# Optimization experiments

Measured on AMD Instinct MI355X. Metric: run time of the kernel, lower is better.

## Reference

```python
import jax, jax.numpy as jnp
import numpy as np

B, N, M, D = 16, 4096, 4096, 3


def setup_inputs() -> dict:
    key = jax.random.key(0)
    k1, k2 = jax.random.split(key)
    xyz1 = jax.random.normal(k1, (B, N, D), dtype=jnp.float32)
    xyz2 = jax.random.normal(k2, (B, M, D), dtype=jnp.float32)
    return {"xyz1": xyz1, "xyz2": xyz2}


def _chamfer(xyz1, xyz2):
    # Squared pairwise distances via ||a||^2 + ||b||^2 - 2 a.b  -> [B, N, M]
    s1 = jnp.sum(xyz1 * xyz1, axis=-1)                     # [B, N]
    s2 = jnp.sum(xyz2 * xyz2, axis=-1)                     # [B, M]
    cross = jnp.einsum("bnd,bmd->bnm", xyz1, xyz2)        # [B, N, M]
    d2 = s1[:, :, None] + s2[:, None, :] - 2.0 * cross
    d2 = jnp.maximum(d2, 0.0)  # guard tiny negatives from cancellation
    dist1 = jnp.min(d2, axis=2)  # nearest point in set2 for each point in set1, [B, N]
    dist2 = jnp.min(d2, axis=1)  # nearest point in set1 for each point in set2, [B, M]
    return dist1, dist2


def reference(xyz1, xyz2):
    return _chamfer(xyz1, xyz2)
```

## Files before the change

### kernel.cpp

```cpp
#include <hip/hip_runtime.h>

typedef _Float16 h8     __attribute__((ext_vector_type(8)));
typedef float    f32x16 __attribute__((ext_vector_type(16)));

#define BB      16
#define NPTS    4096
#define WAVES   4
#define RPW     64
#define RPB     (WAVES * RPW)
#define CSPLIT  2
#define COLS    (NPTS / CSPLIT)
#define CHUNK   256
#define NCHUNK  (COLS / CHUNK)
#define NT      (CHUNK / 32)
#define TPB     (WAVES * 64)

__global__ __launch_bounds__(256) void chamfer_init_out(float* __restrict__ out) {
    int i = blockIdx.x * 256 + threadIdx.x;
    out[i] = 3.0e38f;
}

__global__ __launch_bounds__(TPB, 4) void chamfer_mfma(
    const float* __restrict__ xyz1,
    const float* __restrict__ xyz2,
    float* __restrict__ out)
{
    __shared__ __align__(16) _Float16 sb[2][CHUNK * 16];

    const int tid  = threadIdx.x;
    const int lane = tid & 63;
    const int wv   = tid >> 6;
    const int rb   = blockIdx.x;
    const int b    = blockIdx.y;
    const int z    = blockIdx.z;
    const int dir  = z & 1;
    const int csp  = z >> 1;

    const float* qbase = (dir == 0 ? xyz1 : xyz2) + b * NPTS * 3;
    const float* dbase = (dir == 0 ? xyz2 : xyz1) + b * NPTS * 3 + csp * COLS * 3;

    h8 af0, af1;
#pragma unroll
    for (int rbi = 0; rbi < 2; ++rbi) {
        const int row = rb * RPB + wv * RPW + rbi * 32 + (lane & 31);
        float x = qbase[row * 3 + 0], y = qbase[row * 3 + 1], z2 = qbase[row * 3 + 2];
        float s = fmaf(x, x, fmaf(y, y, z2 * z2));
        _Float16 xh = (_Float16)x, yh = (_Float16)y, zh = (_Float16)z2;
        _Float16 xl = (_Float16)(x - (float)xh);
        _Float16 yl = (_Float16)(y - (float)yh);
        _Float16 zl = (_Float16)(z2 - (float)zh);
        _Float16 sh = (_Float16)s;
        _Float16 sl = (_Float16)(s - (float)sh);
        _Float16 one = (_Float16)1.0f, zero = (_Float16)0.0f;
        h8 a = (lane < 32) ? h8{xh, yh, zh, xh, yh, zh, xl, yl}
                           : h8{zl, sh, sl, one, one, zero, zero, zero};
        if (rbi == 0) af0 = a; else af1 = a;
    }

    const f32x16 Z = {};
    float rm0[16], rm1[16];
#pragma unroll
    for (int r = 0; r < 16; ++r) { rm0[r] = 3.0e38f; rm1[r] = 3.0e38f; }

    const int loff = ((lane >> 5) << 8) + (lane & 31) * 8;

    float vx, vy, vz;
    auto stage_load = [&](int ch) {
        const float* p = dbase + (ch * CHUNK + tid) * 3;
        vx = p[0]; vy = p[1]; vz = p[2];
    };
    auto stage_write = [&](int buf) {
        float s = fmaf(vx, vx, fmaf(vy, vy, vz * vz));
        _Float16 xh = (_Float16)vx, yh = (_Float16)vy, zh = (_Float16)vz;
        _Float16 m2xh = (_Float16)(-2.0f) * xh;
        _Float16 m2yh = (_Float16)(-2.0f) * yh;
        _Float16 m2zh = (_Float16)(-2.0f) * zh;
        _Float16 m2xl = (_Float16)(-2.0f * (vx - (float)xh));
        _Float16 m2yl = (_Float16)(-2.0f * (vy - (float)yh));
        _Float16 m2zl = (_Float16)(-2.0f * (vz - (float)zh));
        _Float16 sh = (_Float16)s;
        _Float16 sl = (_Float16)(s - (float)sh);
        _Float16 one = (_Float16)1.0f, zero = (_Float16)0.0f;
        int off = (tid >> 5) * 512 + (tid & 31) * 8;
        *(h8*)&sb[buf][off]       = h8{m2xh, m2yh, m2zh, m2xl, m2yl, m2zl, m2xh, m2yh};
        *(h8*)&sb[buf][off + 256] = h8{m2zh, one, one, sh, sl, zero, zero, zero};
    };

#define FOLD0(p) _Pragma("unroll") for (int r = 0; r < 16; ++r) rm0[r] = fminf((p)[r], rm0[r]);
#define FOLD1(p) _Pragma("unroll") for (int r = 0; r < 16; ++r) rm1[r] = fminf((p)[r], rm1[r]);

    auto sweep = [&](int buf) {
        const _Float16* base = &sb[buf][0];
        h8 b0 = *(const h8*)(base + loff);
        f32x16 pA0 = __builtin_amdgcn_mfma_f32_32x32x16_f16(af0, b0, Z, 0, 0, 0);
        f32x16 pA1 = __builtin_amdgcn_mfma_f32_32x32x16_f16(af1, b0, Z, 0, 0, 0);
#pragma unroll 1
        for (int t = 1; t + 1 < NT; t += 2) {
            h8 bx = *(const h8*)(base + t * 512 + loff);
            f32x16 pB0 = __builtin_amdgcn_mfma_f32_32x32x16_f16(af0, bx, Z, 0, 0, 0);
            FOLD0(pA0)
            f32x16 pB1 = __builtin_amdgcn_mfma_f32_32x32x16_f16(af1, bx, Z, 0, 0, 0);
            FOLD1(pA1)
            h8 by = *(const h8*)(base + (t + 1) * 512 + loff);
            pA0 = __builtin_amdgcn_mfma_f32_32x32x16_f16(af0, by, Z, 0, 0, 0);
            FOLD0(pB0)
            pA1 = __builtin_amdgcn_mfma_f32_32x32x16_f16(af1, by, Z, 0, 0, 0);
            FOLD1(pB1)
        }
        {
            h8 bx = *(const h8*)(base + (NT - 1) * 512 + loff);
            f32x16 pB0 = __builtin_amdgcn_mfma_f32_32x32x16_f16(af0, bx, Z, 0, 0, 0);
            FOLD0(pA0)
            f32x16 pB1 = __builtin_amdgcn_mfma_f32_32x32x16_f16(af1, bx, Z, 0, 0, 0);
            FOLD1(pA1)
            FOLD0(pB0)
            FOLD1(pB1)
        }
    };

    stage_load(0);
    stage_write(0);
    __syncthreads();
#pragma unroll 1
    for (int ch = 0; ch < NCHUNK; ++ch) {
        int buf = ch & 1;
        if (ch + 1 < NCHUNK) stage_load(ch + 1);
        sweep(buf);
        if (ch + 1 < NCHUNK) stage_write(buf ^ 1);
        __syncthreads();
    }

#pragma unroll
    for (int r = 0; r < 16; ++r) {
        float m = rm0[r];
        m = fminf(m, __shfl_xor(m, 1));
        m = fminf(m, __shfl_xor(m, 2));
        m = fminf(m, __shfl_xor(m, 4));
        m = fminf(m, __shfl_xor(m, 8));
        m = fminf(m, __shfl_xor(m, 16));
        rm0[r] = m;
        float n = rm1[r];
        n = fminf(n, __shfl_xor(n, 1));
        n = fminf(n, __shfl_xor(n, 2));
        n = fminf(n, __shfl_xor(n, 4));
        n = fminf(n, __shfl_xor(n, 8));
        n = fminf(n, __shfl_xor(n, 16));
        rm1[r] = n;
    }
    if ((lane & 31) == 0) {
        const int half = lane >> 5;
        int* o = (int*)out + dir * (BB * NPTS) + b * NPTS + rb * RPB + wv * RPW;
#pragma unroll
        for (int r = 0; r < 16; ++r) {
            int rr = (r & 3) + 8 * (r >> 2) + 4 * half;
            atomicMin(o + rr,      __float_as_int(fmaxf(rm0[r], 0.0f)));
            atomicMin(o + 32 + rr, __float_as_int(fmaxf(rm1[r], 0.0f)));
        }
    }
}

extern "C" void kernel_launch(void* const* d_in, const int* in_sizes, int n_in,
                              void* d_out, int out_size, void* d_ws, size_t ws_size,
                              hipStream_t stream) {
    const float* xyz1 = (const float*)d_in[0];
    const float* xyz2 = (const float*)d_in[1];
    float* out = (float*)d_out;

    hipLaunchKernelGGL(chamfer_init_out, dim3(2 * BB * NPTS / 256), dim3(256), 0, stream, out);

    dim3 grid(NPTS / RPB, BB, 2 * CSPLIT);
    hipLaunchKernelGGL(chamfer_mfma, grid, dim3(TPB), 0, stream, xyz1, xyz2, out);
}
```

Measured before the change: 34.18 us.

## Precompute fp16 operand tiles in prep kernel and stream them with global_load_lds

The fp16 hi/lo operand encoding for both point sets moves into the init kernel, which writes A fragments and B tiles already laid out for LDS into workspace. The main kernel then loads A fragments directly and fills shared memory with asynchronous global_load_lds copies, so per-chunk conversion work disappears from the MFMA loop. The chunk size doubles to 512 and the sweep loop is simplified to four MFMAs followed by a fused min fold. The cost is extra workspace traffic and the loss of the explicit software pipelining between MFMAs and folds.

```diff
diff --git a/kernel.cpp b/kernel.cpp
--- a/kernel.cpp
+++ b/kernel.cpp
@@ -10,19 +10,52 @@
 #define RPB     (WAVES * RPW)
 #define CSPLIT  2
 #define COLS    (NPTS / CSPLIT)
-#define CHUNK   256
+#define CHUNK   512
 #define NCHUNK  (COLS / CHUNK)
 #define NT      (CHUNK / 32)
+#define SEGS    4
 #define TPB     (WAVES * 64)
 
-__global__ __launch_bounds__(256) void chamfer_init_out(float* __restrict__ out) {
-    int i = blockIdx.x * 256 + threadIdx.x;
-    out[i] = 3.0e38f;
+__global__ __launch_bounds__(256) void chamfer_prep(
+    const float* __restrict__ xyz1, const float* __restrict__ xyz2,
+    _Float16* __restrict__ Aws, _Float16* __restrict__ Bws,
+    float* __restrict__ out)
+{
+    const int idx = blockIdx.x * 256 + threadIdx.x;
+    out[idx] = 3.0e38f;
+    const int s   = idx >> 16;
+    const int rem = idx & 65535;
+    const float* p = (s == 0 ? xyz1 : xyz2) + rem * 3;
+    float x = p[0], y = p[1], z = p[2];
+    float ss = fmaf(x, x, fmaf(y, y, z * z));
+    _Float16 xh = (_Float16)x, yh = (_Float16)y, zh = (_Float16)z;
+    _Float16 xl = (_Float16)(x - (float)xh);
+    _Float16 yl = (_Float16)(y - (float)yh);
+    _Float16 zl = (_Float16)(z - (float)zh);
+    _Float16 sh = (_Float16)ss;
+    _Float16 sl = (_Float16)(ss - (float)sh);
+    _Float16 one = (_Float16)1.0f, zero = (_Float16)0.0f;
+    _Float16 m2xh = (_Float16)(-2.0f) * xh;
+    _Float16 m2yh = (_Float16)(-2.0f) * yh;
+    _Float16 m2zh = (_Float16)(-2.0f) * zh;
+    _Float16 m2xl = (_Float16)(-2.0f * (x - (float)xh));
+    _Float16 m2yl = (_Float16)(-2.0f * (y - (float)yh));
+    _Float16 m2zl = (_Float16)(-2.0f * (z - (float)zh));
+
+    _Float16* A = Aws + (size_t)idx * 16;
+    *(h8*)(A)     = h8{xh, yh, zh, xh, yh, zh, xl, yl};
+    *(h8*)(A + 8) = h8{zl, sh, sl, one, one, zero, zero, zero};
+
+    const int pp = idx & 4095;
+    const int slab = idx >> 12;
+    _Float16* B = Bws + (size_t)slab * (NPTS * 16) + (pp >> 5) * 512 + (pp & 31) * 8;
+    *(h8*)(B)       = h8{m2xh, m2yh, m2zh, m2xl, m2yl, m2zl, m2xh, m2yh};
+    *(h8*)(B + 256) = h8{m2zh, one, one, sh, sl, zero, zero, zero};
 }
 
 __global__ __launch_bounds__(TPB, 4) void chamfer_mfma(
-    const float* __restrict__ xyz1,
-    const float* __restrict__ xyz2,
+    const _Float16* __restrict__ Aws,
+    const _Float16* __restrict__ Bws,
     float* __restrict__ out)
 {
     __shared__ __align__(16) _Float16 sb[2][CHUNK * 16];
@@ -36,26 +69,16 @@
     const int dir  = z & 1;
     const int csp  = z >> 1;
 
-    const float* qbase = (dir == 0 ? xyz1 : xyz2) + b * NPTS * 3;
-    const float* dbase = (dir == 0 ? xyz2 : xyz1) + b * NPTS * 3 + csp * COLS * 3;
-
     h8 af0, af1;
-#pragma unroll
-    for (int rbi = 0; rbi < 2; ++rbi) {
-        const int row = rb * RPB + wv * RPW + rbi * 32 + (lane & 31);
-        float x = qbase[row * 3 + 0], y = qbase[row * 3 + 1], z2 = qbase[row * 3 + 2];
-        float s = fmaf(x, x, fmaf(y, y, z2 * z2));
-        _Float16 xh = (_Float16)x, yh = (_Float16)y, zh = (_Float16)z2;
-        _Float16 xl = (_Float16)(x - (float)xh);
-        _Float16 yl = (_Float16)(y - (float)yh);
-        _Float16 zl = (_Float16)(z2 - (float)zh);
-        _Float16 sh = (_Float16)s;
-        _Float16 sl = (_Float16)(s - (float)sh);
-        _Float16 one = (_Float16)1.0f, zero = (_Float16)0.0f;
-        h8 a = (lane < 32) ? h8{xh, yh, zh, xh, yh, zh, xl, yl}
-                           : h8{zl, sh, sl, one, one, zero, zero, zero};
-        if (rbi == 0) af0 = a; else af1 = a;
+    {
+        const _Float16* Abase = Aws + ((size_t)dir << 20) + (size_t)b * (NPTS * 16);
+        const int r0 = rb * RPB + wv * RPW + (lane & 31);
+        const int hs = (lane >> 5) * 8;
+        af0 = *(const h8*)(Abase + (size_t)r0 * 16 + hs);
+        af1 = *(const h8*)(Abase + (size_t)(r0 + 32) * 16 + hs);
     }
+    const _Float16* Bbase = Bws + ((size_t)(dir ^ 1) << 20) + (size_t)b * (NPTS * 16)
+                          + (size_t)csp * (COLS * 16);
 
     const f32x16 Z = {};
     float rm0[16], rm1[16];
@@ -64,69 +87,44 @@
 
     const int loff = ((lane >> 5) << 8) + (lane & 31) * 8;
 
-    float vx, vy, vz;
-    auto stage_load = [&](int ch) {
-        const float* p = dbase + (ch * CHUNK + tid) * 3;
-        vx = p[0]; vy = p[1]; vz = p[2];
+    auto stage = [&](int ch, int buf) {
+        const char* g = (const char*)(Bbase + (size_t)ch * CHUNK * 16);
+        char* l = (char*)&sb[buf][0];
+#pragma unroll
+        for (int j = 0; j < SEGS; ++j) {
+            int seg = wv * SEGS + j;
+            __builtin_amdgcn_global_load_lds(
+                (const unsigned int*)(g + seg * 1024 + lane * 16),
+                (unsigned int*)(l + seg * 1024), 16, 0, 0);
+        }
     };
-    auto stage_write = [&](int buf) {
-        float s = fmaf(vx, vx, fmaf(vy, vy, vz * vz));
-        _Float16 xh = (_Float16)vx, yh = (_Float16)vy, zh = (_Float16)vz;
-        _Float16 m2xh = (_Float16)(-2.0f) * xh;
-        _Float16 m2yh = (_Float16)(-2.0f) * yh;
-        _Float16 m2zh = (_Float16)(-2.0f) * zh;
-        _Float16 m2xl = (_Float16)(-2.0f * (vx - (float)xh));
-        _Float16 m2yl = (_Float16)(-2.0f * (vy - (float)yh));
-        _Float16 m2zl = (_Float16)(-2.0f * (vz - (float)zh));
-        _Float16 sh = (_Float16)s;
-        _Float16 sl = (_Float16)(s - (float)sh);
-        _Float16 one = (_Float16)1.0f, zero = (_Float16)0.0f;
-        int off = (tid >> 5) * 512 + (tid & 31) * 8;
-        *(h8*)&sb[buf][off]       = h8{m2xh, m2yh, m2zh, m2xl, m2yl, m2zl, m2xh, m2yh};
-        *(h8*)&sb[buf][off + 256] = h8{m2zh, one, one, sh, sl, zero, zero, zero};
-    };
-
-#define FOLD0(p) _Pragma("unroll") for (int r = 0; r < 16; ++r) rm0[r] = fminf((p)[r], rm0[r]);
-#define FOLD1(p) _Pragma("unroll") for (int r = 0; r < 16; ++r) rm1[r] = fminf((p)[r], rm1[r]);
 
     auto sweep = [&](int buf) {
         const _Float16* base = &sb[buf][0];
-        h8 b0 = *(const h8*)(base + loff);
-        f32x16 pA0 = __builtin_amdgcn_mfma_f32_32x32x16_f16(af0, b0, Z, 0, 0, 0);
-        f32x16 pA1 = __builtin_amdgcn_mfma_f32_32x32x16_f16(af1, b0, Z, 0, 0, 0);
 #pragma unroll 1
-        for (int t = 1; t + 1 < NT; t += 2) {
+        for (int t = 0; t < NT; t += 2) {
             h8 bx = *(const h8*)(base + t * 512 + loff);
-            f32x16 pB0 = __builtin_amdgcn_mfma_f32_32x32x16_f16(af0, bx, Z, 0, 0, 0);
-            FOLD0(pA0)
-            f32x16 pB1 = __builtin_amdgcn_mfma_f32_32x32x16_f16(af1, bx, Z, 0, 0, 0);
-            FOLD1(pA1)
             h8 by = *(const h8*)(base + (t + 1) * 512 + loff);
-            pA0 = __builtin_amdgcn_mfma_f32_32x32x16_f16(af0, by, Z, 0, 0, 0);
-            FOLD0(pB0)
-            pA1 = __builtin_amdgcn_mfma_f32_32x32x16_f16(af1, by, Z, 0, 0, 0);
-            FOLD1(pB1)
-        }
-        {
-            h8 bx = *(const h8*)(base + (NT - 1) * 512 + loff);
-            f32x16 pB0 = __builtin_amdgcn_mfma_f32_32x32x16_f16(af0, bx, Z, 0, 0, 0);
-            FOLD0(pA0)
-            f32x16 pB1 = __builtin_amdgcn_mfma_f32_32x32x16_f16(af1, bx, Z, 0, 0, 0);
-            FOLD1(pA1)
-            FOLD0(pB0)
-            FOLD1(pB1)
+            f32x16 c0 = __builtin_amdgcn_mfma_f32_32x32x16_f16(af0, bx, Z, 0, 0, 0);
+            f32x16 c1 = __builtin_amdgcn_mfma_f32_32x32x16_f16(af0, by, Z, 0, 0, 0);
+            f32x16 d0 = __builtin_amdgcn_mfma_f32_32x32x16_f16(af1, bx, Z, 0, 0, 0);
+            f32x16 d1 = __builtin_amdgcn_mfma_f32_32x32x16_f16(af1, by, Z, 0, 0, 0);
+#pragma unroll
+            for (int r = 0; r < 16; ++r)
+                rm0[r] = fminf(fminf(c0[r], c1[r]), rm0[r]);
+#pragma unroll
+            for (int r = 0; r < 16; ++r)
+                rm1[r] = fminf(fminf(d0[r], d1[r]), rm1[r]);
         }
     };
 
-    stage_load(0);
-    stage_write(0);
+    stage(0, 0);
     __syncthreads();
 #pragma unroll 1
     for (int ch = 0; ch < NCHUNK; ++ch) {
         int buf = ch & 1;
-        if (ch + 1 < NCHUNK) stage_load(ch + 1);
+        if (ch + 1 < NCHUNK) stage(ch + 1, buf ^ 1);
         sweep(buf);
-        if (ch + 1 < NCHUNK) stage_write(buf ^ 1);
         __syncthreads();
     }
 
@@ -165,9 +163,12 @@
     const float* xyz1 = (const float*)d_in[0];
     const float* xyz2 = (const float*)d_in[1];
     float* out = (float*)d_out;
+    _Float16* Aws = (_Float16*)d_ws;
+    _Float16* Bws = Aws + (size_t)2 * BB * NPTS * 16;
 
-    hipLaunchKernelGGL(chamfer_init_out, dim3(2 * BB * NPTS / 256), dim3(256), 0, stream, out);
+    hipLaunchKernelGGL(chamfer_prep, dim3(2 * BB * NPTS / 256), dim3(256), 0, stream,
+                       xyz1, xyz2, Aws, Bws, out);
 
     dim3 grid(NPTS / RPB, BB, 2 * CSPLIT);
-    hipLaunchKernelGGL(chamfer_mfma, grid, dim3(TPB), 0, stream, xyz1, xyz2, out);
+    hipLaunchKernelGGL(chamfer_mfma, grid, dim3(TPB), 0, stream, Aws, Bws, out);
 }
```

Measured after the change: 36.85 us. +7.8%, slower.
